# Kernel optimization log

Hardware: AMD Instinct MI355X
Metric: run time of the kernel (lower is better)

Reference implementation:

```python
import jax, jax.numpy as jnp
import numpy as np

B, NBC, H, W, HID, OUT = 4, 128, 64, 64, 64, 1
NINT = H * W

def _lin_init(key, fan_in, fan_out):
    kw, kb = jax.random.split(key)
    bound = 1.0 / np.sqrt(fan_in)
    w = jax.random.uniform(kw, (fan_in, fan_out), minval=-bound, maxval=bound, dtype=jnp.float32)
    b = jax.random.uniform(kb, (fan_out,), minval=-bound, maxval=bound, dtype=jnp.float32)
    return w, b

def setup_inputs() -> dict:
    key = jax.random.key(0)
    ks = jax.random.split(key, 7)
    boundary_info = jax.random.normal(ks[0], (B, NBC, 3), dtype=jnp.float32)
    interior_coords = jax.random.uniform(ks[1], (B, NINT, 2), minval=-1.0, maxval=1.0, dtype=jnp.float32)
    W0, b0 = _lin_init(ks[2], 3, HID)        # boundary_encoder layer 0
    W1, b1 = _lin_init(ks[3], HID, HID)      # boundary_encoder layer 1
    G0w, G0b = _lin_init(ks[4], HID + 2, HID)  # green_kernel layer 0
    G1w, G1b = _lin_init(ks[5], HID, HID)      # green_kernel layer 1
    G2w, G2b = _lin_init(ks[6], HID, OUT)      # green_kernel layer 2
    return {"boundary_info": boundary_info, "interior_coords": interior_coords,
            "W0": W0, "b0": b0, "W1": W1, "b1": b1,
            "G0w": G0w, "G0b": G0b, "G1w": G1w, "G1b": G1b,
            "G2w": G2w, "G2b": G2b,
            "interior_h": H, "interior_w": W}

def reference(boundary_info, interior_coords, W0, b0, W1, b1,
              G0w, G0b, G1w, G1b, G2w, G2b, interior_h, interior_w):
    batch, n_bc, _ = boundary_info.shape
    hid = W0.shape[1]
    # boundary encoder: (B, NBC, HID)
    bf = jax.nn.relu(boundary_info @ W0 + b0)
    bf = jax.nn.relu(bf @ W1 + b1)
    # green kernel layer 0: split weight over concat([bf, coords]) so the
    # concatenated (B,NBC,NINT,HID+2) tensor is never materialized.
    a = bf @ G0w[:hid]                      # (B, NBC, HID)
    c = interior_coords @ G0w[hid:]         # (B, NINT, HID)
    h1 = jax.nn.relu(a[:, :, None, :] + c[:, None, :, :] + G0b)  # (B,NBC,NINT,HID)
    h2 = jax.nn.relu(h1 @ G1w + G1b)        # (B, NBC, NINT, HID)
    contribution = h2 @ G2w + G2b           # (B, NBC, NINT, OUT)
    u = contribution.sum(axis=1) / n_bc     # (B, NINT, OUT)
    return u.reshape(batch, 1, interior_h, interior_w)
```

## Files before the change

### kernel.cpp

```cpp
#include <hip/hip_runtime.h>
#include <hip/hip_bf16.h>

#define BB   4
#define NBC  128
#define NINT 4096
#define HID  64

using short8  = __attribute__((ext_vector_type(8)))  short;
using float16 = __attribute__((ext_vector_type(16))) float;
using f2      = __attribute__((ext_vector_type(2)))  float;
using int4v   = __attribute__((ext_vector_type(4)))  int;

static __device__ __forceinline__ short f2bf(float f) {
    __hip_bfloat16 h = __float2bfloat16(f);
    return __builtin_bit_cast(short, h);
}
static __device__ __forceinline__ unsigned fbits(float f) {
    return __builtin_bit_cast(unsigned, f);
}
static __device__ __forceinline__ unsigned pack_bf_trunc(float lo, float hi) {
    return __builtin_amdgcn_perm(fbits(hi), fbits(lo), 0x07060302u);
}

__global__ void __launch_bounds__(256) bge_prep(
    const float* __restrict__ binfo,
    const float* __restrict__ W0,
    const float* __restrict__ b0,
    const float* __restrict__ W1,
    const float* __restrict__ b1,
    const float* __restrict__ G0w,
    const float* __restrict__ G0b,
    float* __restrict__ aprime)
{
    __shared__ float sW1[HID * HID];
    __shared__ float sG0[HID * HID];
    __shared__ float shv [4][HID];
    __shared__ float shv2[4][HID];

    const int tid = threadIdx.x;
    const int wv  = tid >> 6;
    const int t   = tid & 63;
    const int row = blockIdx.x * 4 + wv;

    for (int idx = tid; idx < HID * HID / 4; idx += 256) {
        ((float4*)sW1)[idx] = ((const float4*)W1)[idx];
        ((float4*)sG0)[idx] = ((const float4*)G0w)[idx];
    }

    const float x0 = binfo[row*3+0];
    const float x1 = binfo[row*3+1];
    const float x2 = binfo[row*3+2];
    float h = fmaxf(x0*W0[t] + x1*W0[64+t] + x2*W0[128+t] + b0[t], 0.0f);
    shv[wv][t] = h;
    __syncthreads();

    float acc = b1[t];
    #pragma unroll 8
    for (int k = 0; k < HID; ++k) acc += shv[wv][k] * sW1[k*64 + t];
    shv2[wv][t] = fmaxf(acc, 0.0f);
    __syncthreads();

    float a = G0b[t];
    #pragma unroll 8
    for (int k = 0; k < HID; ++k) a += shv2[wv][k] * sG0[k*64 + t];
    aprime[row*HID + t] = a;
}

__global__ void __launch_bounds__(512) bge_main(
    const float* __restrict__ icoord,
    const float* __restrict__ G0w,
    const float* __restrict__ G1w,
    const float* __restrict__ G1b,
    const float* __restrict__ G2w,
    const float* __restrict__ G2b,
    const float* __restrict__ aprime,
    float* __restrict__ out)
{
    __shared__ __align__(16) float smem[8704 + 512];
    float* const ldsA = smem;
    float* const ldsS = smem;
    float* const red  = smem + 8704;

    const int b    = blockIdx.y;
    const int i0   = blockIdx.x * 32;
    const int tid  = threadIdx.x;
    const int wv   = tid >> 6;
    const int lane = tid & 63;
    const int hf   = lane >> 5;
    const int ln   = lane & 31;

    {
        const float4* src = (const float4*)(aprime + (size_t)b * NBC * HID);
        float4* dst = (float4*)ldsA;
        for (int idx = tid; idx < NBC*HID/4; idx += 512) dst[idx] = src[idx];
    }

    const int i = i0 + ln;
    const float cx = icoord[((size_t)b*NINT + i)*2 + 0];
    const float cy = icoord[((size_t)b*NINT + i)*2 + 1];
    float4 cre4[4][2];
    #pragma unroll
    for (int st = 0; st < 4; ++st)
        #pragma unroll
        for (int h = 0; h < 2; ++h) {
            const int k = st*16 + hf*8 + h*4;
            cre4[st][h] = make_float4(
                cx*G0w[64*64 + k+0] + cy*G0w[65*64 + k+0],
                cx*G0w[64*64 + k+1] + cy*G0w[65*64 + k+1],
                cx*G0w[64*64 + k+2] + cy*G0w[65*64 + k+2],
                cx*G0w[64*64 + k+3] + cy*G0w[65*64 + k+3]);
        }

    short8 bfrag[4][2];
    #pragma unroll
    for (int st = 0; st < 4; ++st)
        #pragma unroll
        for (int t = 0; t < 2; ++t)
            #pragma unroll
            for (int jj = 0; jj < 8; ++jj) {
                const int k = st*16 + hf*8 + jj;
                bfrag[st][t][jj] = f2bf(G1w[k*64 + t*32 + ln]);
            }

    const float b1v0 = G1b[ln],  b1v1 = G1b[32 + ln];
    const float g2v0 = G2w[ln],  g2v1 = G2w[32 + ln];
    const float g2bv = G2b[0];

    const float16 zc = (float16)0.0f;
    f2 s2[8];
    #pragma unroll
    for (int q = 0; q < 8; ++q) s2[q] = (f2)0.0f;

    __syncthreads();

    #pragma unroll 2
    for (int bc = wv*16; bc < wv*16 + 16; ++bc) {
        const float* arow = ldsA + bc*HID;
        float16 acc0, acc1;
        #pragma unroll
        for (int st = 0; st < 4; ++st) {
            const float4* ap4 = (const float4*)(arow + st*16 + hf*8);
            float4 v0 = ap4[0], v1 = ap4[1];
            const float4 c0 = cre4[st][0], c1 = cre4[st][1];
            v0.x = fmaxf(v0.x + c0.x, 0.0f); v0.y = fmaxf(v0.y + c0.y, 0.0f);
            v0.z = fmaxf(v0.z + c0.z, 0.0f); v0.w = fmaxf(v0.w + c0.w, 0.0f);
            v1.x = fmaxf(v1.x + c1.x, 0.0f); v1.y = fmaxf(v1.y + c1.y, 0.0f);
            v1.z = fmaxf(v1.z + c1.z, 0.0f); v1.w = fmaxf(v1.w + c1.w, 0.0f);
            int4v di;
            di[0] = (int)pack_bf_trunc(v0.x, v0.y);
            di[1] = (int)pack_bf_trunc(v0.z, v0.w);
            di[2] = (int)pack_bf_trunc(v1.x, v1.y);
            di[3] = (int)pack_bf_trunc(v1.z, v1.w);
            const short8 af = __builtin_bit_cast(short8, di);
            if (st == 0) {
                acc0 = __builtin_amdgcn_mfma_f32_32x32x16_bf16(af, bfrag[0][0], zc, 0, 0, 0);
                acc1 = __builtin_amdgcn_mfma_f32_32x32x16_bf16(af, bfrag[0][1], zc, 0, 0, 0);
            } else {
                acc0 = __builtin_amdgcn_mfma_f32_32x32x16_bf16(af, bfrag[st][0], acc0, 0, 0, 0);
                acc1 = __builtin_amdgcn_mfma_f32_32x32x16_bf16(af, bfrag[st][1], acc1, 0, 0, 0);
            }
        }
        #pragma unroll
        for (int q = 0; q < 8; ++q) {
            f2 a0; a0[0] = acc0[2*q] + b1v0; a0[1] = acc0[2*q+1] + b1v0;
            f2 a1; a1[0] = acc1[2*q] + b1v1; a1[1] = acc1[2*q+1] + b1v1;
            a0[0] = fmaxf(a0[0], 0.0f); a0[1] = fmaxf(a0[1], 0.0f);
            a1[0] = fmaxf(a1[0], 0.0f); a1[1] = fmaxf(a1[1], 0.0f);
            s2[q] += a0 * g2v0 + a1 * g2v1;
        }
    }

    __syncthreads();

    {
        float* base = ldsS + (wv*64 + lane)*17;
        #pragma unroll
        for (int q = 0; q < 8; ++q) { base[2*q] = s2[q][0]; base[2*q+1] = s2[q][1]; }
    }
    __syncthreads();

    {
        const int m   = tid >> 4;
        const int ch  = tid & 15;
        const int h_m = (m >> 2) & 1;
        const int r_m = (m & 3) | ((m >> 3) << 2);
        const int wvr = ch >> 1;
        const int ln0 = (ch & 1) * 16;
        float acc = 0.0f;
        #pragma unroll
        for (int q = 0; q < 16; ++q)
            acc += ldsS[(wvr*64 + h_m*32 + ln0 + q)*17 + r_m];
        red[m*16 + ch] = acc;
    }
    __syncthreads();

    if (tid < 32) {
        float tot = 0.0f;
        #pragma unroll
        for (int c2 = 0; c2 < 16; ++c2) tot += red[tid*16 + c2];
        out[(size_t)b*NINT + i0 + tid] = tot * (1.0f/128.0f) + g2bv;
    }
}

extern "C" void kernel_launch(void* const* d_in, const int* in_sizes, int n_in,
                              void* d_out, int out_size, void* d_ws, size_t ws_size,
                              hipStream_t stream) {
    const float* binfo  = (const float*)d_in[0];
    const float* icoord = (const float*)d_in[1];
    const float* W0     = (const float*)d_in[2];
    const float* b0     = (const float*)d_in[3];
    const float* W1     = (const float*)d_in[4];
    const float* b1     = (const float*)d_in[5];
    const float* G0w    = (const float*)d_in[6];
    const float* G0b    = (const float*)d_in[7];
    const float* G1w    = (const float*)d_in[8];
    const float* G1b    = (const float*)d_in[9];
    const float* G2w    = (const float*)d_in[10];
    const float* G2b    = (const float*)d_in[11];

    float* aprime = (float*)d_ws;

    hipLaunchKernelGGL(bge_prep, dim3(BB*NBC/4), dim3(256), 0, stream,
                       binfo, W0, b0, W1, b1, G0w, G0b, aprime);
    hipLaunchKernelGGL(bge_main, dim3(NINT/32, BB), dim3(512), 0, stream,
                       icoord, G0w, G1w, G1b, G2w, G2b, aprime,
                       (float*)d_out);
}
```

Baseline: 115.3 us.

## Transpose MFMA operands, fold bias into accumulator, read aprime directly from global

The G1 matmul operands are swapped so the weights become the A operand and activations the B operand, which puts each point's hidden outputs across accumulator rows. The G1 bias is preloaded into the accumulator through a rank-1 MFMA, and the G2 dot product is folded into per-lane scalar sums. The block shrinks to 256 threads with each wave covering 32 boundary rows, the LDS staging of aprime is dropped in favour of direct global (cache) reads, and the final reduction becomes a small 4x64 LDS sum. The intent is to remove LDS staging, the barrier and the transpose-style reduction, at the cost of global-load latency inside the inner loop and less parallelism per block.

```diff
diff --git a/kernel.cpp b/kernel.cpp
--- a/kernel.cpp
+++ b/kernel.cpp
@@ -8,8 +8,6 @@
 
 using short8  = __attribute__((ext_vector_type(8)))  short;
 using float16 = __attribute__((ext_vector_type(16))) float;
-using f2      = __attribute__((ext_vector_type(2)))  float;
-using int4v   = __attribute__((ext_vector_type(4)))  int;
 
 static __device__ __forceinline__ short f2bf(float f) {
     __hip_bfloat16 h = __float2bfloat16(f);
@@ -66,7 +64,7 @@
     aprime[row*HID + t] = a;
 }
 
-__global__ void __launch_bounds__(512) bge_main(
+__global__ void __launch_bounds__(256) bge_main(
     const float* __restrict__ icoord,
     const float* __restrict__ G0w,
     const float* __restrict__ G1w,
@@ -76,10 +74,7 @@
     const float* __restrict__ aprime,
     float* __restrict__ out)
 {
-    __shared__ __align__(16) float smem[8704 + 512];
-    float* const ldsA = smem;
-    float* const ldsS = smem;
-    float* const red  = smem + 8704;
+    __shared__ float sred[4][64];
 
     const int b    = blockIdx.y;
     const int i0   = blockIdx.x * 32;
@@ -89,116 +84,98 @@
     const int hf   = lane >> 5;
     const int ln   = lane & 31;
 
-    {
-        const float4* src = (const float4*)(aprime + (size_t)b * NBC * HID);
-        float4* dst = (float4*)ldsA;
-        for (int idx = tid; idx < NBC*HID/4; idx += 512) dst[idx] = src[idx];
-    }
-
-    const int i = i0 + ln;
-    const float cx = icoord[((size_t)b*NINT + i)*2 + 0];
-    const float cy = icoord[((size_t)b*NINT + i)*2 + 1];
-    float4 cre4[4][2];
+    const float2 cc = ((const float2*)icoord)[(size_t)b*NINT + i0 + ln];
+    float cre[4][8];
     #pragma unroll
     for (int st = 0; st < 4; ++st)
         #pragma unroll
-        for (int h = 0; h < 2; ++h) {
-            const int k = st*16 + hf*8 + h*4;
-            cre4[st][h] = make_float4(
-                cx*G0w[64*64 + k+0] + cy*G0w[65*64 + k+0],
-                cx*G0w[64*64 + k+1] + cy*G0w[65*64 + k+1],
-                cx*G0w[64*64 + k+2] + cy*G0w[65*64 + k+2],
-                cx*G0w[64*64 + k+3] + cy*G0w[65*64 + k+3]);
-        }
-
-    short8 bfrag[4][2];
+        for (int jj = 0; jj < 8; ++jj) {
+            const int k = st*16 + hf*8 + jj;
+            cre[st][jj] = cc.x*G0w[64*64 + k] + cc.y*G0w[65*64 + k];
+        }
+
+    short8 afr[2][4];
     #pragma unroll
-    for (int st = 0; st < 4; ++st)
-        #pragma unroll
-        for (int t = 0; t < 2; ++t)
+    for (int t = 0; t < 2; ++t)
+        #pragma unroll
+        for (int st = 0; st < 4; ++st)
             #pragma unroll
             for (int jj = 0; jj < 8; ++jj) {
                 const int k = st*16 + hf*8 + jj;
-                bfrag[st][t][jj] = f2bf(G1w[k*64 + t*32 + ln]);
+                afr[t][st][jj] = f2bf(G1w[k*64 + t*32 + ln]);
             }
 
-    const float b1v0 = G1b[ln],  b1v1 = G1b[32 + ln];
-    const float g2v0 = G2w[ln],  g2v1 = G2w[32 + ln];
-    const float g2bv = G2b[0];
-
-    const float16 zc = (float16)0.0f;
-    f2 s2[8];
+    float g2c[2][16];
     #pragma unroll
-    for (int q = 0; q < 8; ++q) s2[q] = (f2)0.0f;
-
-    __syncthreads();
-
+    for (int t = 0; t < 2; ++t)
+        #pragma unroll
+        for (int r = 0; r < 16; ++r)
+            g2c[t][r] = G2w[(r&3) + 8*(r>>2) + 4*hf + 32*t];
+
+    float16 accb0, accb1;
+    {
+        short8 afb0 = (short8)0, afb1 = (short8)0, bone = (short8)0;
+        if (hf == 0) {
+            afb0[0] = f2bf(G1b[ln]);
+            afb1[0] = f2bf(G1b[32 + ln]);
+            bone[0] = (short)0x3F80;
+        }
+        const float16 zc = (float16)0.0f;
+        accb0 = __builtin_amdgcn_mfma_f32_32x32x16_bf16(afb0, bone, zc, 0, 0, 0);
+        accb1 = __builtin_amdgcn_mfma_f32_32x32x16_bf16(afb1, bone, zc, 0, 0, 0);
+    }
+
+    float s0 = 0.0f, s1 = 0.0f, s2 = 0.0f, s3 = 0.0f;
+
+    const float* arow = aprime + ((size_t)b*NBC + wv*32)*HID;
     #pragma unroll 2
-    for (int bc = wv*16; bc < wv*16 + 16; ++bc) {
-        const float* arow = ldsA + bc*HID;
-        float16 acc0, acc1;
+    for (int it = 0; it < 32; ++it, arow += HID) {
+        short8 bf[4];
         #pragma unroll
         for (int st = 0; st < 4; ++st) {
-            const float4* ap4 = (const float4*)(arow + st*16 + hf*8);
-            float4 v0 = ap4[0], v1 = ap4[1];
-            const float4 c0 = cre4[st][0], c1 = cre4[st][1];
-            v0.x = fmaxf(v0.x + c0.x, 0.0f); v0.y = fmaxf(v0.y + c0.y, 0.0f);
-            v0.z = fmaxf(v0.z + c0.z, 0.0f); v0.w = fmaxf(v0.w + c0.w, 0.0f);
-            v1.x = fmaxf(v1.x + c1.x, 0.0f); v1.y = fmaxf(v1.y + c1.y, 0.0f);
-            v1.z = fmaxf(v1.z + c1.z, 0.0f); v1.w = fmaxf(v1.w + c1.w, 0.0f);
-            int4v di;
-            di[0] = (int)pack_bf_trunc(v0.x, v0.y);
-            di[1] = (int)pack_bf_trunc(v0.z, v0.w);
-            di[2] = (int)pack_bf_trunc(v1.x, v1.y);
-            di[3] = (int)pack_bf_trunc(v1.z, v1.w);
-            const short8 af = __builtin_bit_cast(short8, di);
-            if (st == 0) {
-                acc0 = __builtin_amdgcn_mfma_f32_32x32x16_bf16(af, bfrag[0][0], zc, 0, 0, 0);
-                acc1 = __builtin_amdgcn_mfma_f32_32x32x16_bf16(af, bfrag[0][1], zc, 0, 0, 0);
-            } else {
-                acc0 = __builtin_amdgcn_mfma_f32_32x32x16_bf16(af, bfrag[st][0], acc0, 0, 0, 0);
-                acc1 = __builtin_amdgcn_mfma_f32_32x32x16_bf16(af, bfrag[st][1], acc1, 0, 0, 0);
-            }
-        }
-        #pragma unroll
-        for (int q = 0; q < 8; ++q) {
-            f2 a0; a0[0] = acc0[2*q] + b1v0; a0[1] = acc0[2*q+1] + b1v0;
-            f2 a1; a1[0] = acc1[2*q] + b1v1; a1[1] = acc1[2*q+1] + b1v1;
-            a0[0] = fmaxf(a0[0], 0.0f); a0[1] = fmaxf(a0[1], 0.0f);
-            a1[0] = fmaxf(a1[0], 0.0f); a1[1] = fmaxf(a1[1], 0.0f);
-            s2[q] += a0 * g2v0 + a1 * g2v1;
-        }
-    }
-
-    __syncthreads();
-
-    {
-        float* base = ldsS + (wv*64 + lane)*17;
-        #pragma unroll
-        for (int q = 0; q < 8; ++q) { base[2*q] = s2[q][0]; base[2*q+1] = s2[q][1]; }
-    }
-    __syncthreads();
-
-    {
-        const int m   = tid >> 4;
-        const int ch  = tid & 15;
-        const int h_m = (m >> 2) & 1;
-        const int r_m = (m & 3) | ((m >> 3) << 2);
-        const int wvr = ch >> 1;
-        const int ln0 = (ch & 1) * 16;
-        float acc = 0.0f;
-        #pragma unroll
-        for (int q = 0; q < 16; ++q)
-            acc += ldsS[(wvr*64 + h_m*32 + ln0 + q)*17 + r_m];
-        red[m*16 + ch] = acc;
-    }
+            const float4 v0 = *(const float4*)(arow + st*16 + hf*8);
+            const float4 v1 = *(const float4*)(arow + st*16 + hf*8 + 4);
+            const float e0 = fmaxf(v0.x + cre[st][0], 0.0f);
+            const float e1 = fmaxf(v0.y + cre[st][1], 0.0f);
+            const float e2 = fmaxf(v0.z + cre[st][2], 0.0f);
+            const float e3 = fmaxf(v0.w + cre[st][3], 0.0f);
+            const float e4 = fmaxf(v1.x + cre[st][4], 0.0f);
+            const float e5 = fmaxf(v1.y + cre[st][5], 0.0f);
+            const float e6 = fmaxf(v1.z + cre[st][6], 0.0f);
+            const float e7 = fmaxf(v1.w + cre[st][7], 0.0f);
+            int di0 = (int)pack_bf_trunc(e0, e1);
+            int di1 = (int)pack_bf_trunc(e2, e3);
+            int di2 = (int)pack_bf_trunc(e4, e5);
+            int di3 = (int)pack_bf_trunc(e6, e7);
+            bf[st][0] = (short)(di0 & 0xFFFF); bf[st][1] = (short)(((unsigned)di0) >> 16);
+            bf[st][2] = (short)(di1 & 0xFFFF); bf[st][3] = (short)(((unsigned)di1) >> 16);
+            bf[st][4] = (short)(di2 & 0xFFFF); bf[st][5] = (short)(((unsigned)di2) >> 16);
+            bf[st][6] = (short)(di3 & 0xFFFF); bf[st][7] = (short)(((unsigned)di3) >> 16);
+        }
+        float16 acc0 = __builtin_amdgcn_mfma_f32_32x32x16_bf16(afr[0][0], bf[0], accb0, 0, 0, 0);
+        float16 acc1 = __builtin_amdgcn_mfma_f32_32x32x16_bf16(afr[1][0], bf[0], accb1, 0, 0, 0);
+        #pragma unroll
+        for (int st = 1; st < 4; ++st) {
+            acc0 = __builtin_amdgcn_mfma_f32_32x32x16_bf16(afr[0][st], bf[st], acc0, 0, 0, 0);
+            acc1 = __builtin_amdgcn_mfma_f32_32x32x16_bf16(afr[1][st], bf[st], acc1, 0, 0, 0);
+        }
+        #pragma unroll
+        for (int r = 0; r < 16; r += 4) {
+            s0 += fmaxf(acc0[r+0], 0.0f)*g2c[0][r+0] + fmaxf(acc1[r+0], 0.0f)*g2c[1][r+0];
+            s1 += fmaxf(acc0[r+1], 0.0f)*g2c[0][r+1] + fmaxf(acc1[r+1], 0.0f)*g2c[1][r+1];
+            s2 += fmaxf(acc0[r+2], 0.0f)*g2c[0][r+2] + fmaxf(acc1[r+2], 0.0f)*g2c[1][r+2];
+            s3 += fmaxf(acc0[r+3], 0.0f)*g2c[0][r+3] + fmaxf(acc1[r+3], 0.0f)*g2c[1][r+3];
+        }
+    }
+
+    sred[wv][lane] = (s0 + s1) + (s2 + s3);
     __syncthreads();
 
     if (tid < 32) {
         float tot = 0.0f;
         #pragma unroll
-        for (int c2 = 0; c2 < 16; ++c2) tot += red[tid*16 + c2];
-        out[(size_t)b*NINT + i0 + tid] = tot * (1.0f/128.0f) + g2bv;
+        for (int w = 0; w < 4; ++w) tot += sred[w][tid] + sred[w][tid + 32];
+        out[(size_t)b*NINT + i0 + tid] = tot * (1.0f/128.0f) + G2b[0];
     }
 }
 
@@ -222,7 +199,7 @@
 
     hipLaunchKernelGGL(bge_prep, dim3(BB*NBC/4), dim3(256), 0, stream,
                        binfo, W0, b0, W1, b1, G0w, G0b, aprime);
-    hipLaunchKernelGGL(bge_main, dim3(NINT/32, BB), dim3(512), 0, stream,
+    hipLaunchKernelGGL(bge_main, dim3(NINT/32, BB), dim3(256), 0, stream,
                        icoord, G0w, G1w, G1b, G2w, G2b, aprime,
                        (float*)d_out);
 }
```

Result: slower. 123.2 us (+6.8%).

## Split boundary reduction across two blocks with atomic accumulation

Applied to the files above, without the earlier changes.

The main kernel grid gets a z dimension of 2, so each block handles 64 of the 128 boundary points and adds its partial sum into the output with atomicAdd. The output is zeroed in the prep kernel. This doubles the block count (512 to 1024) for more parallelism and halves the per-block LDS staging and serial loop length, at the cost of recomputing coordinate and weight fragments in both halves and adding atomics. It also folds the bias add into the ReLU by clamping against the negated bias and adding a bias-times-weight correction once after the loop, which saves a VALU add per element.

```diff
diff --git a/kernel.cpp b/kernel.cpp
--- a/kernel.cpp
+++ b/kernel.cpp
@@ -30,7 +30,8 @@
     const float* __restrict__ b1,
     const float* __restrict__ G0w,
     const float* __restrict__ G0b,
-    float* __restrict__ aprime)
+    float* __restrict__ aprime,
+    float* __restrict__ out)
 {
     __shared__ float sW1[HID * HID];
     __shared__ float sG0[HID * HID];
@@ -41,6 +42,9 @@
     const int wv  = tid >> 6;
     const int t   = tid & 63;
     const int row = blockIdx.x * 4 + wv;
+
+    const int g = blockIdx.x * 256 + tid;
+    if (g < BB * NINT) out[g] = 0.0f;
 
     for (int idx = tid; idx < HID * HID / 4; idx += 256) {
         ((float4*)sW1)[idx] = ((const float4*)W1)[idx];
@@ -83,6 +87,7 @@
 
     const int b    = blockIdx.y;
     const int i0   = blockIdx.x * 32;
+    const int zh   = blockIdx.z;
     const int tid  = threadIdx.x;
     const int wv   = tid >> 6;
     const int lane = tid & 63;
@@ -90,14 +95,13 @@
     const int ln   = lane & 31;
 
     {
-        const float4* src = (const float4*)(aprime + (size_t)b * NBC * HID);
+        const float4* src = (const float4*)(aprime + ((size_t)b*NBC + zh*64) * HID);
         float4* dst = (float4*)ldsA;
-        for (int idx = tid; idx < NBC*HID/4; idx += 512) dst[idx] = src[idx];
-    }
-
-    const int i = i0 + ln;
-    const float cx = icoord[((size_t)b*NINT + i)*2 + 0];
-    const float cy = icoord[((size_t)b*NINT + i)*2 + 1];
+        #pragma unroll
+        for (int idx = tid; idx < 64*HID/4; idx += 512) dst[idx] = src[idx];
+    }
+
+    const float2 cc = ((const float2*)icoord)[(size_t)b*NINT + i0 + ln];
     float4 cre4[4][2];
     #pragma unroll
     for (int st = 0; st < 4; ++st)
@@ -105,10 +109,10 @@
         for (int h = 0; h < 2; ++h) {
             const int k = st*16 + hf*8 + h*4;
             cre4[st][h] = make_float4(
-                cx*G0w[64*64 + k+0] + cy*G0w[65*64 + k+0],
-                cx*G0w[64*64 + k+1] + cy*G0w[65*64 + k+1],
-                cx*G0w[64*64 + k+2] + cy*G0w[65*64 + k+2],
-                cx*G0w[64*64 + k+3] + cy*G0w[65*64 + k+3]);
+                cc.x*G0w[64*64 + k+0] + cc.y*G0w[65*64 + k+0],
+                cc.x*G0w[64*64 + k+1] + cc.y*G0w[65*64 + k+1],
+                cc.x*G0w[64*64 + k+2] + cc.y*G0w[65*64 + k+2],
+                cc.x*G0w[64*64 + k+3] + cc.y*G0w[65*64 + k+3]);
         }
 
     short8 bfrag[4][2];
@@ -124,7 +128,7 @@
 
     const float b1v0 = G1b[ln],  b1v1 = G1b[32 + ln];
     const float g2v0 = G2w[ln],  g2v1 = G2w[32 + ln];
-    const float g2bv = G2b[0];
+    const float nb0 = -b1v0, nb1 = -b1v1;
 
     const float16 zc = (float16)0.0f;
     f2 s2[8];
@@ -133,9 +137,9 @@
 
     __syncthreads();
 
+    const float* arow = ldsA + (wv*8)*HID;
     #pragma unroll 2
-    for (int bc = wv*16; bc < wv*16 + 16; ++bc) {
-        const float* arow = ldsA + bc*HID;
+    for (int it = 0; it < 8; ++it, arow += HID) {
         float16 acc0, acc1;
         #pragma unroll
         for (int st = 0; st < 4; ++st) {
@@ -162,12 +166,17 @@
         }
         #pragma unroll
         for (int q = 0; q < 8; ++q) {
-            f2 a0; a0[0] = acc0[2*q] + b1v0; a0[1] = acc0[2*q+1] + b1v0;
-            f2 a1; a1[0] = acc1[2*q] + b1v1; a1[1] = acc1[2*q+1] + b1v1;
-            a0[0] = fmaxf(a0[0], 0.0f); a0[1] = fmaxf(a0[1], 0.0f);
-            a1[0] = fmaxf(a1[0], 0.0f); a1[1] = fmaxf(a1[1], 0.0f);
+            f2 a0, a1;
+            a0[0] = fmaxf(acc0[2*q],   nb0); a0[1] = fmaxf(acc0[2*q+1], nb0);
+            a1[0] = fmaxf(acc1[2*q],   nb1); a1[1] = fmaxf(acc1[2*q+1], nb1);
             s2[q] += a0 * g2v0 + a1 * g2v1;
         }
+    }
+
+    {
+        const float corr = 8.0f * (b1v0 * g2v0 + b1v1 * g2v1);
+        #pragma unroll
+        for (int q = 0; q < 8; ++q) { s2[q][0] += corr; s2[q][1] += corr; }
     }
 
     __syncthreads();
@@ -198,7 +207,8 @@
         float tot = 0.0f;
         #pragma unroll
         for (int c2 = 0; c2 < 16; ++c2) tot += red[tid*16 + c2];
-        out[(size_t)b*NINT + i0 + tid] = tot * (1.0f/128.0f) + g2bv;
+        atomicAdd(out + (size_t)b*NINT + i0 + tid,
+                  tot * (1.0f/128.0f) + 0.5f * G2b[0]);
     }
 }
 
@@ -221,8 +231,8 @@
     float* aprime = (float*)d_ws;
 
     hipLaunchKernelGGL(bge_prep, dim3(BB*NBC/4), dim3(256), 0, stream,
-                       binfo, W0, b0, W1, b1, G0w, G0b, aprime);
-    hipLaunchKernelGGL(bge_main, dim3(NINT/32, BB), dim3(512), 0, stream,
+                       binfo, W0, b0, W1, b1, G0w, G0b, aprime, (float*)d_out);
+    hipLaunchKernelGGL(bge_main, dim3(NINT/32, BB, 2), dim3(512), 0, stream,
                        icoord, G0w, G1w, G1b, G2w, G2b, aprime,
                        (float*)d_out);
 }
```

New measurement: 125.5 us. 1.09x slower.
